# Kernel tuning notes

Hardware: AMD Instinct MI355X
Metric: run time of the kernel (lower is better)

Reference implementation:

```python
import jax, jax.numpy as jnp
import numpy as np

N_HEAD = 16
ROPE_THETA = 10000.0


def setup_inputs() -> dict:
    key = jax.random.key(0)
    k0, k1, k2 = jax.random.split(key, 3)
    B, T, C = 2, 2048, 1024
    s = 0.02  # GPT-2 style init scale
    return {
        "x": jax.random.normal(k0, (B, T, C), jnp.float32),
        "w_attn": jax.random.normal(k1, (C, 3 * C), jnp.float32) * s,
        "b_attn": jnp.zeros((3 * C,), jnp.float32),
        "w_proj": jax.random.normal(k2, (C, C), jnp.float32) * s,
        "b_proj": jnp.zeros((C,), jnp.float32),
    }


def _rope(x):
    # x: [B, H, T, D]; interleaved-pair rotary (lucidrains rotate_queries_or_keys)
    T, D = x.shape[-2], x.shape[-1]
    inv_freq = 1.0 / (ROPE_THETA ** (jnp.arange(0, D, 2, dtype=jnp.float32) / D))
    freqs = jnp.arange(T, dtype=jnp.float32)[:, None] * inv_freq[None, :]  # [T, D/2]
    emb = jnp.repeat(freqs, 2, axis=-1)  # [T, D], each freq duplicated per pair
    cos, sin = jnp.cos(emb), jnp.sin(emb)
    xr = x.reshape(*x.shape[:-1], D // 2, 2)
    x1, x2 = xr[..., 0], xr[..., 1]
    rot = jnp.stack((-x2, x1), axis=-1).reshape(x.shape)  # rotate_half
    return x * cos + rot * sin


def reference(x, w_attn, b_attn, w_proj, b_proj):
    B, T, C = x.shape
    H = N_HEAD
    D = C // H
    qkv = x @ w_attn + b_attn                      # [B, T, 3C]
    q, k, v = jnp.split(qkv, 3, axis=-1)

    def heads(t):
        return t.reshape(B, T, H, D).transpose(0, 2, 1, 3)  # [B, H, T, D]

    q, k, v = heads(q), heads(k), heads(v)
    q = _rope(q)
    k = _rope(k)

    att = jnp.einsum("bhqd,bhkd->bhqk", q, k) * (1.0 / np.sqrt(D))
    causal = jnp.tril(jnp.ones((T, T), dtype=bool))
    att = jnp.where(causal, att, -jnp.inf)
    att = jax.nn.softmax(att, axis=-1)
    y = jnp.einsum("bhqk,bhkd->bhqd", att, v)
    y = y.transpose(0, 2, 1, 3).reshape(B, T, C)
    return y @ w_proj + b_proj
```

## Files before the change

kernel.cpp:

```cpp
#include <hip/hip_runtime.h>
#include <hip/hip_bf16.h>
#include <stdint.h>

typedef __hip_bfloat16 bf16;
typedef __attribute__((ext_vector_type(8))) short bf16x8;
typedef __attribute__((ext_vector_type(4))) float f32x4;

__device__ inline float bf2f(bf16 v) { return __bfloat162float(v); }
__device__ inline bf16 f2bf(float f) { return __float2bfloat16(f); }

__device__ inline void glds16(const void* g, void* l) {
    __builtin_amdgcn_global_load_lds(
        (const __attribute__((address_space(1))) uint32_t*)g,
        (__attribute__((address_space(3))) uint32_t*)l, 16, 0, 0);
}

__global__ __launch_bounds__(256) void conv_x(const float* __restrict__ in,
                                              bf16* __restrict__ out)
{
    size_t i = ((size_t)blockIdx.x * 256 + threadIdx.x) * 8;
    float4 f0 = *(const float4*)(in + i);
    float4 f1 = *(const float4*)(in + i + 4);
    union { bf16x8 v; bf16 e[8]; } u;
    u.e[0] = f2bf(f0.x); u.e[1] = f2bf(f0.y); u.e[2] = f2bf(f0.z); u.e[3] = f2bf(f0.w);
    u.e[4] = f2bf(f1.x); u.e[5] = f2bf(f1.y); u.e[6] = f2bf(f1.z); u.e[7] = f2bf(f1.w);
    *(bf16x8*)(out + i) = u.v;
}

__global__ __launch_bounds__(256) void conv_wt(const float* __restrict__ W,
                                               bf16* __restrict__ Wt, int N, int K)
{
    __shared__ bf16 t[64][72];
    const int n0 = blockIdx.x * 64, k0 = blockIdx.y * 64;
    const int tid = threadIdx.x;
#pragma unroll
    for (int p = 0; p < 4; ++p) {
        int idx = p * 256 + tid;
        int kr = idx >> 4, c4 = idx & 15;
        float4 f = *(const float4*)(W + (size_t)(k0 + kr) * N + n0 + c4 * 4);
        t[kr][c4 * 4 + 0] = f2bf(f.x); t[kr][c4 * 4 + 1] = f2bf(f.y);
        t[kr][c4 * 4 + 2] = f2bf(f.z); t[kr][c4 * 4 + 3] = f2bf(f.w);
    }
    __syncthreads();
#pragma unroll
    for (int p = 0; p < 2; ++p) {
        int idx = p * 256 + tid;
        int nr = idx >> 3, ch = idx & 7;
        union { bf16x8 v; bf16 e[8]; } u;
#pragma unroll
        for (int j = 0; j < 8; ++j) u.e[j] = t[ch * 8 + j][nr];
        *(bf16x8*)(Wt + (size_t)(n0 + nr) * K + k0 + ch * 8) = u.v;
    }
}

template <bool OUTF32>
__global__ __launch_bounds__(256) void gemm_bt(
    const bf16* __restrict__ A, const bf16* __restrict__ Bt,
    const float* __restrict__ bias, int M, int N, int K, void* __restrict__ outv)
{
    __shared__ __align__(16) bf16 sa[128 * 32];
    __shared__ __align__(16) bf16 sb[128 * 32];

    const int tid  = threadIdx.x;
    const int wave = tid >> 6, lane = tid & 63;
    const int quad = lane >> 4, l16 = lane & 15;
    const int wm = wave >> 1, wn = wave & 1;
    const int row0 = blockIdx.x * 128, n0 = blockIdx.y * 128;

    f32x4 acc[4][4] = {};

    const int sm = wave * 16 + (lane >> 2);
    const int sk = (lane & 3) * 8;
    const bf16* ga = A  + (size_t)(row0 + sm) * K + sk;
    const bf16* gb = Bt + (size_t)(n0  + sm) * K + sk;
    bf16* la = sa + wave * 512;
    bf16* lb = sb + wave * 512;

    for (int k0 = 0; k0 < K; k0 += 32) {
        __syncthreads();
        glds16(ga + k0, la);
        glds16(ga + k0 + (size_t)64 * K, la + 2048);
        glds16(gb + k0, lb);
        glds16(gb + k0 + (size_t)64 * K, lb + 2048);
        __syncthreads();

        bf16x8 af[4], bfr[4];
#pragma unroll
        for (int mi = 0; mi < 4; ++mi)
            af[mi] = *(const bf16x8*)&sa[(wm * 64 + mi * 16 + l16) * 32 + quad * 8];
#pragma unroll
        for (int ni = 0; ni < 4; ++ni)
            bfr[ni] = *(const bf16x8*)&sb[(wn * 64 + ni * 16 + l16) * 32 + quad * 8];
#pragma unroll
        for (int mi = 0; mi < 4; ++mi)
#pragma unroll
            for (int ni = 0; ni < 4; ++ni)
                acc[mi][ni] = __builtin_amdgcn_mfma_f32_16x16x32_bf16(
                    af[mi], bfr[ni], acc[mi][ni], 0, 0, 0);
    }

#pragma unroll
    for (int ni = 0; ni < 4; ++ni) {
        int col = n0 + wn * 64 + ni * 16 + l16;
        float bvv = bias[col];
#pragma unroll
        for (int mi = 0; mi < 4; ++mi) {
#pragma unroll
            for (int r = 0; r < 4; ++r) {
                int row = row0 + wm * 64 + mi * 16 + quad * 4 + r;
                float v = acc[mi][ni][r] + bvv;
                if (OUTF32) ((float*)outv)[(size_t)row * N + col] = v;
                else        ((bf16*)outv)[(size_t)row * N + col] = f2bf(v);
            }
        }
    }
}

__global__ __launch_bounds__(256) void rope_k(
    const bf16* __restrict__ qkv, bf16* __restrict__ q, bf16* __restrict__ k)
{
    int gid = blockIdx.x * 256 + threadIdx.x;
    int p  = gid & 31, d0 = p * 2;
    int t  = (gid >> 5) & 2047;
    int h  = (gid >> 16) & 15;
    int b  = gid >> 20;

    size_t src = ((size_t)(b * 2048 + t)) * 3072 + h * 64 + d0;
    size_t dst = (((size_t)(b * 16 + h)) * 2048 + t) * 64 + d0;

    float invf = expf(-(float)d0 * (9.210340371976184f / 64.0f));
    float sn, cs;
    sincosf((float)t * invf, &sn, &cs);

    float q0 = bf2f(qkv[src]),        q1 = bf2f(qkv[src + 1]);
    float k0 = bf2f(qkv[src + 1024]), k1 = bf2f(qkv[src + 1025]);
    q[dst]     = f2bf((q0 * cs - q1 * sn) * 0.125f);
    q[dst + 1] = f2bf((q1 * cs + q0 * sn) * 0.125f);
    k[dst]     = f2bf(k0 * cs - k1 * sn);
    k[dst + 1] = f2bf(k1 * cs + k0 * sn);
}

__global__ __launch_bounds__(256) void transpose_v(
    const bf16* __restrict__ qkv, bf16* __restrict__ vt)
{
    __shared__ bf16 t[64][72];
    const int t0 = blockIdx.x * 64;
    const int bh = blockIdx.y, b = bh >> 4, h = bh & 15;
    const int tid = threadIdx.x;
#pragma unroll
    for (int p = 0; p < 2; ++p) {
        int idx = p * 256 + tid;
        int tr = idx >> 3, ch = idx & 7;
        bf16x8 v = *(const bf16x8*)(qkv + ((size_t)(b * 2048 + t0 + tr)) * 3072
                                    + 2048 + h * 64 + ch * 8);
#pragma unroll
        for (int j = 0; j < 8; ++j) t[tr][ch * 8 + j] = ((const bf16*)&v)[j];
    }
    __syncthreads();
#pragma unroll
    for (int p = 0; p < 2; ++p) {
        int idx = p * 256 + tid;
        int dr = idx >> 3, ch = idx & 7;
        union { bf16x8 v; bf16 e[8]; } u;
#pragma unroll
        for (int j = 0; j < 8; ++j) u.e[j] = t[ch * 8 + j][dr];
        *(bf16x8*)(vt + ((size_t)bh * 64 + dr) * 2048 + t0 + ch * 8) = u.v;
    }
}

__global__ __launch_bounds__(256) void attn_k(
    const bf16* __restrict__ qg, const bf16* __restrict__ kg,
    const bf16* __restrict__ vtg, bf16* __restrict__ y)
{
    __shared__ __align__(16) bf16 sK[128 * 64];
    __shared__ __align__(16) bf16 sV[64 * 128];
    __shared__ __align__(16) bf16 pL[4][16][136];

    const int tid  = threadIdx.x;
    const int wave = tid >> 6, lane = tid & 63;
    const int quad = lane >> 4, l16 = lane & 15;
    const int bh   = blockIdx.x;
    const int pair = blockIdx.y;
    const bf16* Q  = qg  + (size_t)bh * 2048 * 64;
    const bf16* K  = kg  + (size_t)bh * 2048 * 64;
    const bf16* Vt = vtg + (size_t)bh * 64 * 2048;
    const int b = bh >> 4, h = bh & 15;

    for (int half = 0; half < 2; ++half) {
        const int qt = half ? (31 - pair) : pair;
        const int q0 = qt * 64 + wave * 16;

        bf16x8 aq[2];
        aq[0] = *(const bf16x8*)(Q + (size_t)(q0 + l16) * 64 + quad * 8);
        aq[1] = *(const bf16x8*)(Q + (size_t)(q0 + l16) * 64 + 32 + quad * 8);

        f32x4 o[4] = {};
        float m_r[4] = {-1e30f, -1e30f, -1e30f, -1e30f};
        float l_r[4] = {0.f, 0.f, 0.f, 0.f};

        for (int kt = 0; kt <= q0 + 15; kt += 128) {
            __syncthreads();
#pragma unroll
            for (int c = 0; c < 4; ++c) {
                int key = wave * 32 + c * 8 + (lane >> 3);
                int p = lane & 7;
                glds16(K + (size_t)(kt + key) * 64 + ((p ^ key) & 7) * 8,
                       &sK[(wave * 32 + c * 8) * 64]);
            }
#pragma unroll
            for (int c = 0; c < 4; ++c) {
                int d = wave * 16 + c * 4 + (lane >> 4);
                int p = lane & 15;
                glds16(Vt + (size_t)d * 2048 + kt + ((p ^ d) & 15) * 8,
                       &sV[(wave * 16 + c * 4) * 128]);
            }
            __syncthreads();

            const int nlast = min(7, (q0 - kt) >> 4);
            f32x4 sc[8];
#pragma unroll
            for (int nt = 0; nt < 8; ++nt) {
                if (nt > nlast) continue;
                int key = nt * 16 + l16;
                f32x4 s0 = {};
                bf16x8 bk0 = *(const bf16x8*)&sK[key * 64 + ((quad ^ key) & 7) * 8];
                s0 = __builtin_amdgcn_mfma_f32_16x16x32_bf16(aq[0], bk0, s0, 0, 0, 0);
                bf16x8 bk1 = *(const bf16x8*)&sK[key * 64 + (((4 + quad) ^ key) & 7) * 8];
                sc[nt] = __builtin_amdgcn_mfma_f32_16x16x32_bf16(aq[1], bk1, s0, 0, 0, 0);
            }
            {
                const int diag = (q0 - kt) >> 4;
                if (diag <= 7) {
                    int key = kt + diag * 16 + l16;
#pragma unroll
                    for (int r = 0; r < 4; ++r) {
                        int row = q0 + quad * 4 + r;
                        if (key > row) sc[diag][r] = -1e30f;
                    }
                }
            }
            float rowmax[4] = {-1e30f, -1e30f, -1e30f, -1e30f};
#pragma unroll
            for (int nt = 0; nt < 8; ++nt) {
                if (nt > nlast) continue;
#pragma unroll
                for (int r = 0; r < 4; ++r) rowmax[r] = fmaxf(rowmax[r], sc[nt][r]);
            }
#pragma unroll
            for (int off = 1; off < 16; off <<= 1)
#pragma unroll
                for (int r = 0; r < 4; ++r)
                    rowmax[r] = fmaxf(rowmax[r], __shfl_xor(rowmax[r], off));

            float alpha[4];
#pragma unroll
            for (int r = 0; r < 4; ++r) {
                float mn = fmaxf(m_r[r], rowmax[r]);
                alpha[r] = __expf(m_r[r] - mn);
                m_r[r] = mn;
            }
            float rs[4] = {0.f, 0.f, 0.f, 0.f};
#pragma unroll
            for (int nt = 0; nt < 8; ++nt) {
                if (nt > nlast) continue;
#pragma unroll
                for (int r = 0; r < 4; ++r) {
                    float p = __expf(sc[nt][r] - m_r[r]);
                    sc[nt][r] = p;
                    rs[r] += p;
                }
            }
#pragma unroll
            for (int off = 1; off < 16; off <<= 1)
#pragma unroll
                for (int r = 0; r < 4; ++r) rs[r] += __shfl_xor(rs[r], off);
#pragma unroll
            for (int r = 0; r < 4; ++r) l_r[r] = l_r[r] * alpha[r] + rs[r];
#pragma unroll
            for (int nt = 0; nt < 4; ++nt)
#pragma unroll
                for (int r = 0; r < 4; ++r) o[nt][r] *= alpha[r];

#pragma unroll
            for (int nt = 0; nt < 8; ++nt) {
                if (nt > nlast) continue;
                int blk = (2 * nt + (l16 >> 3)) ^ quad;
#pragma unroll
                for (int r = 0; r < 4; ++r)
                    pL[wave][quad * 4 + r][blk * 8 + (l16 & 7)] = f2bf(sc[nt][r]);
            }
            if (nlast < 7 && !(nlast & 1)) {
                int blk = (2 * (nlast + 1) + (l16 >> 3)) ^ quad;
#pragma unroll
                for (int r = 0; r < 4; ++r)
                    pL[wave][quad * 4 + r][blk * 8 + (l16 & 7)] = f2bf(0.f);
            }
#pragma unroll
            for (int c = 0; c < 4; ++c) {
                if (c > (nlast >> 1)) continue;
                bf16x8 pa = *(const bf16x8*)&pL[wave][l16][(((4 * c + quad) ^ (l16 >> 2)) * 8)];
#pragma unroll
                for (int dnt = 0; dnt < 4; ++dnt) {
                    int d = dnt * 16 + l16;
                    int cc = c * 4 + quad;
                    bf16x8 vb = *(const bf16x8*)&sV[d * 128 + ((cc ^ d) & 15) * 8];
                    o[dnt] = __builtin_amdgcn_mfma_f32_16x16x32_bf16(pa, vb, o[dnt], 0, 0, 0);
                }
            }
        }

#pragma unroll
        for (int r = 0; r < 4; ++r) {
            float inv = 1.0f / l_r[r];
            int qq = q0 + quad * 4 + r;
#pragma unroll
            for (int nt = 0; nt < 4; ++nt) {
                int d = nt * 16 + l16;
                y[((size_t)(b * 2048 + qq)) * 1024 + h * 64 + d] = f2bf(o[nt][r] * inv);
            }
        }
    }
}

extern "C" void kernel_launch(void* const* d_in, const int* in_sizes, int n_in,
                              void* d_out, int out_size, void* d_ws, size_t ws_size,
                              hipStream_t stream) {
    const float* x      = (const float*)d_in[0];
    const float* w_attn = (const float*)d_in[1];
    const float* b_attn = (const float*)d_in[2];
    const float* w_proj = (const float*)d_in[3];
    const float* b_proj = (const float*)d_in[4];
    float* out = (float*)d_out;

    bf16* xbf = (bf16*)d_ws;
    bf16* wat = xbf + (size_t)4194304;
    bf16* wpt = wat + (size_t)3145728;
    bf16* qkv = wpt + (size_t)1048576;
    bf16* qh  = qkv + (size_t)12582912;
    bf16* kh  = qh  + (size_t)4194304;
    bf16* vt  = kh  + (size_t)4194304;
    bf16* yws = vt  + (size_t)4194304;

    dim3 blk(256);
    conv_x<<<dim3(2048), blk, 0, stream>>>(x, xbf);
    conv_wt<<<dim3(48, 16), blk, 0, stream>>>(w_attn, wat, 3072, 1024);
    conv_wt<<<dim3(16, 16), blk, 0, stream>>>(w_proj, wpt, 1024, 1024);
    gemm_bt<false><<<dim3(32, 24), blk, 0, stream>>>(xbf, wat, b_attn,
                                                     4096, 3072, 1024, qkv);
    rope_k<<<dim3(8192), blk, 0, stream>>>(qkv, qh, kh);
    transpose_v<<<dim3(32, 32), blk, 0, stream>>>(qkv, vt);
    attn_k<<<dim3(32, 16), blk, 0, stream>>>(qh, kh, vt, yws);
    gemm_bt<true><<<dim3(32, 8), blk, 0, stream>>>(yws, wpt, b_proj,
                                                   4096, 1024, 1024, out);
    (void)in_sizes; (void)n_in; (void)ws_size; (void)out_size;
}
```

Before: 234.0 us.

## Drop LDS staging in attention, read K/V from global, one tile per block

```diff
diff --git a/kernel.cpp b/kernel.cpp
--- a/kernel.cpp
+++ b/kernel.cpp
@@ -132,10 +132,11 @@
     float sn, cs;
     sincosf((float)t * invf, &sn, &cs);
 
+    const float QS = 0.125f * 1.44269504088896f;
     float q0 = bf2f(qkv[src]),        q1 = bf2f(qkv[src + 1]);
     float k0 = bf2f(qkv[src + 1024]), k1 = bf2f(qkv[src + 1025]);
-    q[dst]     = f2bf((q0 * cs - q1 * sn) * 0.125f);
-    q[dst + 1] = f2bf((q1 * cs + q0 * sn) * 0.125f);
+    q[dst]     = f2bf((q0 * cs - q1 * sn) * QS);
+    q[dst + 1] = f2bf((q1 * cs + q0 * sn) * QS);
     k[dst]     = f2bf(k0 * cs - k1 * sn);
     k[dst + 1] = f2bf(k1 * cs + k0 * sn);
 }
@@ -172,152 +173,134 @@
     const bf16* __restrict__ qg, const bf16* __restrict__ kg,
     const bf16* __restrict__ vtg, bf16* __restrict__ y)
 {
-    __shared__ __align__(16) bf16 sK[128 * 64];
-    __shared__ __align__(16) bf16 sV[64 * 128];
     __shared__ __align__(16) bf16 pL[4][16][136];
 
     const int tid  = threadIdx.x;
     const int wave = tid >> 6, lane = tid & 63;
     const int quad = lane >> 4, l16 = lane & 15;
     const int bh   = blockIdx.x;
-    const int pair = blockIdx.y;
+    const int qt   = 31 - blockIdx.y;
     const bf16* Q  = qg  + (size_t)bh * 2048 * 64;
     const bf16* K  = kg  + (size_t)bh * 2048 * 64;
     const bf16* Vt = vtg + (size_t)bh * 64 * 2048;
     const int b = bh >> 4, h = bh & 15;
 
-    for (int half = 0; half < 2; ++half) {
-        const int qt = half ? (31 - pair) : pair;
-        const int q0 = qt * 64 + wave * 16;
-
-        bf16x8 aq[2];
-        aq[0] = *(const bf16x8*)(Q + (size_t)(q0 + l16) * 64 + quad * 8);
-        aq[1] = *(const bf16x8*)(Q + (size_t)(q0 + l16) * 64 + 32 + quad * 8);
-
-        f32x4 o[4] = {};
-        float m_r[4] = {-1e30f, -1e30f, -1e30f, -1e30f};
-        float l_r[4] = {0.f, 0.f, 0.f, 0.f};
-
-        for (int kt = 0; kt <= q0 + 15; kt += 128) {
-            __syncthreads();
-#pragma unroll
-            for (int c = 0; c < 4; ++c) {
-                int key = wave * 32 + c * 8 + (lane >> 3);
-                int p = lane & 7;
-                glds16(K + (size_t)(kt + key) * 64 + ((p ^ key) & 7) * 8,
-                       &sK[(wave * 32 + c * 8) * 64]);
-            }
-#pragma unroll
-            for (int c = 0; c < 4; ++c) {
-                int d = wave * 16 + c * 4 + (lane >> 4);
-                int p = lane & 15;
-                glds16(Vt + (size_t)d * 2048 + kt + ((p ^ d) & 15) * 8,
-                       &sV[(wave * 16 + c * 4) * 128]);
-            }
-            __syncthreads();
-
-            const int nlast = min(7, (q0 - kt) >> 4);
-            f32x4 sc[8];
-#pragma unroll
-            for (int nt = 0; nt < 8; ++nt) {
-                if (nt > nlast) continue;
-                int key = nt * 16 + l16;
-                f32x4 s0 = {};
-                bf16x8 bk0 = *(const bf16x8*)&sK[key * 64 + ((quad ^ key) & 7) * 8];
-                s0 = __builtin_amdgcn_mfma_f32_16x16x32_bf16(aq[0], bk0, s0, 0, 0, 0);
-                bf16x8 bk1 = *(const bf16x8*)&sK[key * 64 + (((4 + quad) ^ key) & 7) * 8];
-                sc[nt] = __builtin_amdgcn_mfma_f32_16x16x32_bf16(aq[1], bk1, s0, 0, 0, 0);
-            }
-            {
-                const int diag = (q0 - kt) >> 4;
-                if (diag <= 7) {
-                    int key = kt + diag * 16 + l16;
-#pragma unroll
-                    for (int r = 0; r < 4; ++r) {
-                        int row = q0 + quad * 4 + r;
-                        if (key > row) sc[diag][r] = -1e30f;
-                    }
+    const int q0 = qt * 64 + wave * 16;
+
+    bf16x8 aq[2];
+    aq[0] = *(const bf16x8*)(Q + (size_t)(q0 + l16) * 64 + quad * 8);
+    aq[1] = *(const bf16x8*)(Q + (size_t)(q0 + l16) * 64 + 32 + quad * 8);
+
+    f32x4 o[4] = {};
+    float m_r[4] = {-1e30f, -1e30f, -1e30f, -1e30f};
+    float l_r[4] = {0.f, 0.f, 0.f, 0.f};
+
+    for (int kt = 0; kt <= q0 + 15; kt += 128) {
+        const int nlast = min(7, (q0 - kt) >> 4);
+        f32x4 sc[8];
+        __builtin_amdgcn_s_setprio(1);
+#pragma unroll
+        for (int nt = 0; nt < 8; ++nt) {
+            if (nt > nlast) continue;
+            const bf16* kp = K + (size_t)(kt + nt * 16 + l16) * 64;
+            bf16x8 bk0 = *(const bf16x8*)(kp + quad * 8);
+            bf16x8 bk1 = *(const bf16x8*)(kp + 32 + quad * 8);
+            f32x4 s0 = {};
+            s0 = __builtin_amdgcn_mfma_f32_16x16x32_bf16(aq[0], bk0, s0, 0, 0, 0);
+            sc[nt] = __builtin_amdgcn_mfma_f32_16x16x32_bf16(aq[1], bk1, s0, 0, 0, 0);
+        }
+        __builtin_amdgcn_s_setprio(0);
+        {
+            const int diag = (q0 - kt) >> 4;
+            if (diag <= 7) {
+                int key = kt + diag * 16 + l16;
+#pragma unroll
+                for (int r = 0; r < 4; ++r) {
+                    int row = q0 + quad * 4 + r;
+                    if (key > row) sc[diag][r] = -1e30f;
                 }
             }
-            float rowmax[4] = {-1e30f, -1e30f, -1e30f, -1e30f};
-#pragma unroll
-            for (int nt = 0; nt < 8; ++nt) {
-                if (nt > nlast) continue;
-#pragma unroll
-                for (int r = 0; r < 4; ++r) rowmax[r] = fmaxf(rowmax[r], sc[nt][r]);
+        }
+        float rowmax[4] = {-1e30f, -1e30f, -1e30f, -1e30f};
+#pragma unroll
+        for (int nt = 0; nt < 8; ++nt) {
+            if (nt > nlast) continue;
+#pragma unroll
+            for (int r = 0; r < 4; ++r) rowmax[r] = fmaxf(rowmax[r], sc[nt][r]);
+        }
+#pragma unroll
+        for (int off = 1; off < 16; off <<= 1)
+#pragma unroll
+            for (int r = 0; r < 4; ++r)
+                rowmax[r] = fmaxf(rowmax[r], __shfl_xor(rowmax[r], off));
+
+        float alpha[4];
+#pragma unroll
+        for (int r = 0; r < 4; ++r) {
+            float mn = fmaxf(m_r[r], rowmax[r]);
+            alpha[r] = exp2f(m_r[r] - mn);
+            m_r[r] = mn;
+        }
+        float rs[4] = {0.f, 0.f, 0.f, 0.f};
+#pragma unroll
+        for (int nt = 0; nt < 8; ++nt) {
+            if (nt > nlast) continue;
+#pragma unroll
+            for (int r = 0; r < 4; ++r) {
+                float p = exp2f(sc[nt][r] - m_r[r]);
+                sc[nt][r] = p;
+                rs[r] += p;
             }
-#pragma unroll
-            for (int off = 1; off < 16; off <<= 1)
-#pragma unroll
-                for (int r = 0; r < 4; ++r)
-                    rowmax[r] = fmaxf(rowmax[r], __shfl_xor(rowmax[r], off));
-
-            float alpha[4];
-#pragma unroll
-            for (int r = 0; r < 4; ++r) {
-                float mn = fmaxf(m_r[r], rowmax[r]);
-                alpha[r] = __expf(m_r[r] - mn);
-                m_r[r] = mn;
+        }
+#pragma unroll
+        for (int off = 1; off < 16; off <<= 1)
+#pragma unroll
+            for (int r = 0; r < 4; ++r) rs[r] += __shfl_xor(rs[r], off);
+#pragma unroll
+        for (int r = 0; r < 4; ++r) l_r[r] = l_r[r] * alpha[r] + rs[r];
+#pragma unroll
+        for (int nt = 0; nt < 4; ++nt)
+#pragma unroll
+            for (int r = 0; r < 4; ++r) o[nt][r] *= alpha[r];
+
+#pragma unroll
+        for (int nt = 0; nt < 8; ++nt) {
+            if (nt > nlast) continue;
+            int blk = (2 * nt + (l16 >> 3)) ^ quad;
+#pragma unroll
+            for (int r = 0; r < 4; ++r)
+                pL[wave][quad * 4 + r][blk * 8 + (l16 & 7)] = f2bf(sc[nt][r]);
+        }
+        if (nlast < 7 && !(nlast & 1)) {
+            int blk = (2 * (nlast + 1) + (l16 >> 3)) ^ quad;
+#pragma unroll
+            for (int r = 0; r < 4; ++r)
+                pL[wave][quad * 4 + r][blk * 8 + (l16 & 7)] = f2bf(0.f);
+        }
+        __builtin_amdgcn_s_setprio(1);
+#pragma unroll
+        for (int c = 0; c < 4; ++c) {
+            if (c > (nlast >> 1)) continue;
+            bf16x8 pa = *(const bf16x8*)&pL[wave][l16][(((4 * c + quad) ^ (l16 >> 2)) * 8)];
+#pragma unroll
+            for (int dnt = 0; dnt < 4; ++dnt) {
+                int d = dnt * 16 + l16;
+                bf16x8 vb = *(const bf16x8*)(Vt + (size_t)d * 2048 + kt
+                                             + (c * 4 + quad) * 8);
+                o[dnt] = __builtin_amdgcn_mfma_f32_16x16x32_bf16(pa, vb, o[dnt], 0, 0, 0);
             }
-            float rs[4] = {0.f, 0.f, 0.f, 0.f};
-#pragma unroll
-            for (int nt = 0; nt < 8; ++nt) {
-                if (nt > nlast) continue;
-#pragma unroll
-                for (int r = 0; r < 4; ++r) {
-                    float p = __expf(sc[nt][r] - m_r[r]);
-                    sc[nt][r] = p;
-                    rs[r] += p;
-                }
-            }
-#pragma unroll
-            for (int off = 1; off < 16; off <<= 1)
-#pragma unroll
-                for (int r = 0; r < 4; ++r) rs[r] += __shfl_xor(rs[r], off);
-#pragma unroll
-            for (int r = 0; r < 4; ++r) l_r[r] = l_r[r] * alpha[r] + rs[r];
-#pragma unroll
-            for (int nt = 0; nt < 4; ++nt)
-#pragma unroll
-                for (int r = 0; r < 4; ++r) o[nt][r] *= alpha[r];
-
-#pragma unroll
-            for (int nt = 0; nt < 8; ++nt) {
-                if (nt > nlast) continue;
-                int blk = (2 * nt + (l16 >> 3)) ^ quad;
-#pragma unroll
-                for (int r = 0; r < 4; ++r)
-                    pL[wave][quad * 4 + r][blk * 8 + (l16 & 7)] = f2bf(sc[nt][r]);
-            }
-            if (nlast < 7 && !(nlast & 1)) {
-                int blk = (2 * (nlast + 1) + (l16 >> 3)) ^ quad;
-#pragma unroll
-                for (int r = 0; r < 4; ++r)
-                    pL[wave][quad * 4 + r][blk * 8 + (l16 & 7)] = f2bf(0.f);
-            }
-#pragma unroll
-            for (int c = 0; c < 4; ++c) {
-                if (c > (nlast >> 1)) continue;
-                bf16x8 pa = *(const bf16x8*)&pL[wave][l16][(((4 * c + quad) ^ (l16 >> 2)) * 8)];
-#pragma unroll
-                for (int dnt = 0; dnt < 4; ++dnt) {
-                    int d = dnt * 16 + l16;
-                    int cc = c * 4 + quad;
-                    bf16x8 vb = *(const bf16x8*)&sV[d * 128 + ((cc ^ d) & 15) * 8];
-                    o[dnt] = __builtin_amdgcn_mfma_f32_16x16x32_bf16(pa, vb, o[dnt], 0, 0, 0);
-                }
-            }
-        }
-
-#pragma unroll
-        for (int r = 0; r < 4; ++r) {
-            float inv = 1.0f / l_r[r];
-            int qq = q0 + quad * 4 + r;
-#pragma unroll
-            for (int nt = 0; nt < 4; ++nt) {
-                int d = nt * 16 + l16;
-                y[((size_t)(b * 2048 + qq)) * 1024 + h * 64 + d] = f2bf(o[nt][r] * inv);
-            }
+        }
+        __builtin_amdgcn_s_setprio(0);
+    }
+
+#pragma unroll
+    for (int r = 0; r < 4; ++r) {
+        float inv = 1.0f / l_r[r];
+        int qq = q0 + quad * 4 + r;
+#pragma unroll
+        for (int nt = 0; nt < 4; ++nt) {
+            int d = nt * 16 + l16;
+            y[((size_t)(b * 2048 + qq)) * 1024 + h * 64 + d] = f2bf(o[nt][r] * inv);
         }
     }
 }
@@ -349,7 +332,7 @@
                                                      4096, 3072, 1024, qkv);
     rope_k<<<dim3(8192), blk, 0, stream>>>(qkv, qh, kh);
     transpose_v<<<dim3(32, 32), blk, 0, stream>>>(qkv, vt);
-    attn_k<<<dim3(32, 16), blk, 0, stream>>>(qh, kh, vt, yws);
+    attn_k<<<dim3(32, 32), blk, 0, stream>>>(qh, kh, vt, yws);
     gemm_bt<true><<<dim3(32, 8), blk, 0, stream>>>(yws, wpt, b_proj,
                                                    4096, 1024, 1024, out);
     (void)in_sizes; (void)n_in; (void)ws_size; (void)out_size;
```

Result: slower. 298.0 us (+27.4%).

## Restructure attention softmax: exp2 scaling, lazy rescale, MFMA row sums, one tile per block

Applied to the files above, without the earlier changes.

```diff
diff --git a/kernel.cpp b/kernel.cpp
--- a/kernel.cpp
+++ b/kernel.cpp
@@ -132,10 +132,11 @@
     float sn, cs;
     sincosf((float)t * invf, &sn, &cs);
 
+    const float QS = 0.125f * 1.44269504088896f;
     float q0 = bf2f(qkv[src]),        q1 = bf2f(qkv[src + 1]);
     float k0 = bf2f(qkv[src + 1024]), k1 = bf2f(qkv[src + 1025]);
-    q[dst]     = f2bf((q0 * cs - q1 * sn) * 0.125f);
-    q[dst + 1] = f2bf((q1 * cs + q0 * sn) * 0.125f);
+    q[dst]     = f2bf((q0 * cs - q1 * sn) * QS);
+    q[dst + 1] = f2bf((q1 * cs + q0 * sn) * QS);
     k[dst]     = f2bf(k0 * cs - k1 * sn);
     k[dst + 1] = f2bf(k1 * cs + k0 * sn);
 }
@@ -180,144 +181,146 @@
     const int wave = tid >> 6, lane = tid & 63;
     const int quad = lane >> 4, l16 = lane & 15;
     const int bh   = blockIdx.x;
-    const int pair = blockIdx.y;
+    const int qt   = 31 - (int)blockIdx.y;
     const bf16* Q  = qg  + (size_t)bh * 2048 * 64;
     const bf16* K  = kg  + (size_t)bh * 2048 * 64;
     const bf16* Vt = vtg + (size_t)bh * 64 * 2048;
     const int b = bh >> 4, h = bh & 15;
 
-    for (int half = 0; half < 2; ++half) {
-        const int qt = half ? (31 - pair) : pair;
-        const int q0 = qt * 64 + wave * 16;
-
-        bf16x8 aq[2];
-        aq[0] = *(const bf16x8*)(Q + (size_t)(q0 + l16) * 64 + quad * 8);
-        aq[1] = *(const bf16x8*)(Q + (size_t)(q0 + l16) * 64 + 32 + quad * 8);
-
-        f32x4 o[4] = {};
-        float m_r[4] = {-1e30f, -1e30f, -1e30f, -1e30f};
-        float l_r[4] = {0.f, 0.f, 0.f, 0.f};
-
-        for (int kt = 0; kt <= q0 + 15; kt += 128) {
-            __syncthreads();
-#pragma unroll
-            for (int c = 0; c < 4; ++c) {
-                int key = wave * 32 + c * 8 + (lane >> 3);
-                int p = lane & 7;
-                glds16(K + (size_t)(kt + key) * 64 + ((p ^ key) & 7) * 8,
-                       &sK[(wave * 32 + c * 8) * 64]);
-            }
-#pragma unroll
-            for (int c = 0; c < 4; ++c) {
-                int d = wave * 16 + c * 4 + (lane >> 4);
-                int p = lane & 15;
-                glds16(Vt + (size_t)d * 2048 + kt + ((p ^ d) & 15) * 8,
-                       &sV[(wave * 16 + c * 4) * 128]);
-            }
-            __syncthreads();
-
-            const int nlast = min(7, (q0 - kt) >> 4);
-            f32x4 sc[8];
-#pragma unroll
-            for (int nt = 0; nt < 8; ++nt) {
-                if (nt > nlast) continue;
-                int key = nt * 16 + l16;
-                f32x4 s0 = {};
-                bf16x8 bk0 = *(const bf16x8*)&sK[key * 64 + ((quad ^ key) & 7) * 8];
-                s0 = __builtin_amdgcn_mfma_f32_16x16x32_bf16(aq[0], bk0, s0, 0, 0, 0);
-                bf16x8 bk1 = *(const bf16x8*)&sK[key * 64 + (((4 + quad) ^ key) & 7) * 8];
-                sc[nt] = __builtin_amdgcn_mfma_f32_16x16x32_bf16(aq[1], bk1, s0, 0, 0, 0);
-            }
-            {
-                const int diag = (q0 - kt) >> 4;
-                if (diag <= 7) {
-                    int key = kt + diag * 16 + l16;
-#pragma unroll
-                    for (int r = 0; r < 4; ++r) {
-                        int row = q0 + quad * 4 + r;
-                        if (key > row) sc[diag][r] = -1e30f;
-                    }
+    const int q0 = qt * 64 + wave * 16;
+
+    bf16x8 aq[2];
+    aq[0] = *(const bf16x8*)(Q + (size_t)(q0 + l16) * 64 + quad * 8);
+    aq[1] = *(const bf16x8*)(Q + (size_t)(q0 + l16) * 64 + 32 + quad * 8);
+
+    union { bf16x8 v; short e[8]; } uo;
+#pragma unroll
+    for (int j = 0; j < 8; ++j) uo.e[j] = (short)0x3F80;
+    const bf16x8 vones = uo.v;
+
+    f32x4 o[4] = {};
+    f32x4 ls   = {};
+    float m_r[4] = {-1e30f, -1e30f, -1e30f, -1e30f};
+    const float THR = 8.0f;
+
+    for (int kt = 0; kt <= q0 + 15; kt += 128) {
+        __syncthreads();
+#pragma unroll
+        for (int c = 0; c < 4; ++c) {
+            int key = wave * 32 + c * 8 + (lane >> 3);
+            int p = lane & 7;
+            glds16(K + (size_t)(kt + key) * 64 + ((p ^ key) & 7) * 8,
+                   &sK[(wave * 32 + c * 8) * 64]);
+        }
+#pragma unroll
+        for (int c = 0; c < 4; ++c) {
+            int d = wave * 16 + c * 4 + (lane >> 4);
+            int p = lane & 15;
+            glds16(Vt + (size_t)d * 2048 + kt + ((p ^ d) & 15) * 8,
+                   &sV[(wave * 16 + c * 4) * 128]);
+        }
+        __syncthreads();
+
+        const int nlast = min(7, (q0 - kt) >> 4);
+        f32x4 sc[8];
+        __builtin_amdgcn_s_setprio(1);
+#pragma unroll
+        for (int nt = 0; nt < 8; ++nt) {
+            if (nt > nlast) continue;
+            int key = nt * 16 + l16;
+            f32x4 s0 = {};
+            bf16x8 bk0 = *(const bf16x8*)&sK[key * 64 + ((quad ^ key) & 7) * 8];
+            s0 = __builtin_amdgcn_mfma_f32_16x16x32_bf16(aq[0], bk0, s0, 0, 0, 0);
+            bf16x8 bk1 = *(const bf16x8*)&sK[key * 64 + (((4 + quad) ^ key) & 7) * 8];
+            sc[nt] = __builtin_amdgcn_mfma_f32_16x16x32_bf16(aq[1], bk1, s0, 0, 0, 0);
+        }
+        __builtin_amdgcn_s_setprio(0);
+        {
+            const int diag = (q0 - kt) >> 4;
+            if (diag <= 7) {
+                int key = kt + diag * 16 + l16;
+#pragma unroll
+                for (int r = 0; r < 4; ++r) {
+                    int row = q0 + quad * 4 + r;
+                    if (key > row) sc[diag][r] = -1e30f;
                 }
             }
-            float rowmax[4] = {-1e30f, -1e30f, -1e30f, -1e30f};
-#pragma unroll
-            for (int nt = 0; nt < 8; ++nt) {
-                if (nt > nlast) continue;
-#pragma unroll
-                for (int r = 0; r < 4; ++r) rowmax[r] = fmaxf(rowmax[r], sc[nt][r]);
-            }
+        }
+        float rowmax[4] = {-1e30f, -1e30f, -1e30f, -1e30f};
+#pragma unroll
+        for (int nt = 0; nt < 8; ++nt) {
+            if (nt > nlast) continue;
+#pragma unroll
+            for (int r = 0; r < 4; ++r) rowmax[r] = fmaxf(rowmax[r], sc[nt][r]);
+        }
+        bool okl = (rowmax[0] <= m_r[0] + THR) && (rowmax[1] <= m_r[1] + THR) &&
+                   (rowmax[2] <= m_r[2] + THR) && (rowmax[3] <= m_r[3] + THR);
+        if (!__all((int)okl)) {
 #pragma unroll
             for (int off = 1; off < 16; off <<= 1)
 #pragma unroll
                 for (int r = 0; r < 4; ++r)
                     rowmax[r] = fmaxf(rowmax[r], __shfl_xor(rowmax[r], off));
-
             float alpha[4];
 #pragma unroll
             for (int r = 0; r < 4; ++r) {
                 float mn = fmaxf(m_r[r], rowmax[r]);
-                alpha[r] = __expf(m_r[r] - mn);
+                alpha[r] = exp2f(m_r[r] - mn);
                 m_r[r] = mn;
             }
-            float rs[4] = {0.f, 0.f, 0.f, 0.f};
-#pragma unroll
-            for (int nt = 0; nt < 8; ++nt) {
-                if (nt > nlast) continue;
-#pragma unroll
-                for (int r = 0; r < 4; ++r) {
-                    float p = __expf(sc[nt][r] - m_r[r]);
-                    sc[nt][r] = p;
-                    rs[r] += p;
-                }
+#pragma unroll
+            for (int nt = 0; nt < 4; ++nt)
+#pragma unroll
+                for (int r = 0; r < 4; ++r) o[nt][r] *= alpha[r];
+#pragma unroll
+            for (int r = 0; r < 4; ++r) ls[r] *= alpha[r];
+        }
+#pragma unroll
+        for (int nt = 0; nt < 8; ++nt) {
+            if (nt > nlast) continue;
+#pragma unroll
+            for (int r = 0; r < 4; ++r) sc[nt][r] = exp2f(sc[nt][r] - m_r[r]);
+        }
+
+#pragma unroll
+        for (int nt = 0; nt < 8; ++nt) {
+            if (nt > nlast) continue;
+            int blk = (2 * nt + (l16 >> 3)) ^ quad;
+#pragma unroll
+            for (int r = 0; r < 4; ++r)
+                pL[wave][quad * 4 + r][blk * 8 + (l16 & 7)] = f2bf(sc[nt][r]);
+        }
+        if (nlast < 7 && !(nlast & 1)) {
+            int blk = (2 * (nlast + 1) + (l16 >> 3)) ^ quad;
+#pragma unroll
+            for (int r = 0; r < 4; ++r)
+                pL[wave][quad * 4 + r][blk * 8 + (l16 & 7)] = f2bf(0.f);
+        }
+        __builtin_amdgcn_s_setprio(1);
+#pragma unroll
+        for (int c = 0; c < 4; ++c) {
+            if (c > (nlast >> 1)) continue;
+            bf16x8 pa = *(const bf16x8*)&pL[wave][l16][(((4 * c + quad) ^ (l16 >> 2)) * 8)];
+            ls = __builtin_amdgcn_mfma_f32_16x16x32_bf16(pa, vones, ls, 0, 0, 0);
+#pragma unroll
+            for (int dnt = 0; dnt < 4; ++dnt) {
+                int d = dnt * 16 + l16;
+                int cc = c * 4 + quad;
+                bf16x8 vb = *(const bf16x8*)&sV[d * 128 + ((cc ^ d) & 15) * 8];
+                o[dnt] = __builtin_amdgcn_mfma_f32_16x16x32_bf16(pa, vb, o[dnt], 0, 0, 0);
             }
-#pragma unroll
-            for (int off = 1; off < 16; off <<= 1)
-#pragma unroll
-                for (int r = 0; r < 4; ++r) rs[r] += __shfl_xor(rs[r], off);
-#pragma unroll
-            for (int r = 0; r < 4; ++r) l_r[r] = l_r[r] * alpha[r] + rs[r];
-#pragma unroll
-            for (int nt = 0; nt < 4; ++nt)
-#pragma unroll
-                for (int r = 0; r < 4; ++r) o[nt][r] *= alpha[r];
-
-#pragma unroll
-            for (int nt = 0; nt < 8; ++nt) {
-                if (nt > nlast) continue;
-                int blk = (2 * nt + (l16 >> 3)) ^ quad;
-#pragma unroll
-                for (int r = 0; r < 4; ++r)
-                    pL[wave][quad * 4 + r][blk * 8 + (l16 & 7)] = f2bf(sc[nt][r]);
-            }
-            if (nlast < 7 && !(nlast & 1)) {
-                int blk = (2 * (nlast + 1) + (l16 >> 3)) ^ quad;
-#pragma unroll
-                for (int r = 0; r < 4; ++r)
-                    pL[wave][quad * 4 + r][blk * 8 + (l16 & 7)] = f2bf(0.f);
-            }
-#pragma unroll
-            for (int c = 0; c < 4; ++c) {
-                if (c > (nlast >> 1)) continue;
-                bf16x8 pa = *(const bf16x8*)&pL[wave][l16][(((4 * c + quad) ^ (l16 >> 2)) * 8)];
-#pragma unroll
-                for (int dnt = 0; dnt < 4; ++dnt) {
-                    int d = dnt * 16 + l16;
-                    int cc = c * 4 + quad;
-                    bf16x8 vb = *(const bf16x8*)&sV[d * 128 + ((cc ^ d) & 15) * 8];
-                    o[dnt] = __builtin_amdgcn_mfma_f32_16x16x32_bf16(pa, vb, o[dnt], 0, 0, 0);
-                }
-            }
-        }
-
-#pragma unroll
-        for (int r = 0; r < 4; ++r) {
-            float inv = 1.0f / l_r[r];
-            int qq = q0 + quad * 4 + r;
-#pragma unroll
-            for (int nt = 0; nt < 4; ++nt) {
-                int d = nt * 16 + l16;
-                y[((size_t)(b * 2048 + qq)) * 1024 + h * 64 + d] = f2bf(o[nt][r] * inv);
-            }
+        }
+        __builtin_amdgcn_s_setprio(0);
+    }
+
+#pragma unroll
+    for (int r = 0; r < 4; ++r) {
+        float inv = 1.0f / ls[r];
+        int qq = q0 + quad * 4 + r;
+#pragma unroll
+        for (int nt = 0; nt < 4; ++nt) {
+            int d = nt * 16 + l16;
+            y[((size_t)(b * 2048 + qq)) * 1024 + h * 64 + d] = f2bf(o[nt][r] * inv);
         }
     }
 }
@@ -349,7 +352,7 @@
                                                      4096, 3072, 1024, qkv);
     rope_k<<<dim3(8192), blk, 0, stream>>>(qkv, qh, kh);
     transpose_v<<<dim3(32, 32), blk, 0, stream>>>(qkv, vt);
-    attn_k<<<dim3(32, 16), blk, 0, stream>>>(qh, kh, vt, yws);
+    attn_k<<<dim3(32, 32), blk, 0, stream>>>(qh, kh, vt, yws);
     gemm_bt<true><<<dim3(32, 8), blk, 0, stream>>>(yws, wpt, b_proj,
                                                    4096, 1024, 1024, out);
     (void)in_sizes; (void)n_in; (void)ws_size; (void)out_size;
```

Result: faster. 226.2 us (-3.3%).
